# Kernel tuning notes

Measured on AMD Instinct MI355X. Metric: run time of the kernel, lower is better.

The kernel has to match this reference:

```python
import jax, jax.numpy as jnp
import numpy as np

QMIN, QMAX = 0.0, 255.0  # uint8 activation quantization range


def _qlinear(x, w_q, b, s_in, zp_in, s_w):
    """zentorch_qlinear: quantize fp32 x to uint8, int8 weight, dequant output.

    x:   [M, K] fp32
    w_q: [N, K] int8 values (stored int32), symmetric (weight zp = 0)
    b:   [N] fp32
    s_in, zp_in: scalars (activation scale / zero point)
    s_w: [N] per-output-channel weight scales
    """
    zp = zp_in.astype(jnp.float32)
    q = jnp.clip(jnp.round(x / s_in) + zp, QMIN, QMAX)      # fake-quant uint8
    x_dq = (q - zp) * s_in                                   # dequantized activation
    w_dq = w_q.astype(jnp.float32) * s_w[:, None]            # [N, K] dequant weight
    return x_dq @ w_dq.T + b                                 # [M, N] fp32


def setup_inputs() -> dict:
    key = jax.random.key(0)
    k1, k2, k3, k4 = jax.random.split(key, 4)
    M, K, N = 8192, 4096, 4096
    inp = {
        "input": jax.random.normal(k1, (M, K), dtype=jnp.float32),
        "weights": jax.random.randint(k2, (N, K), -128, 128, dtype=jnp.int32),
        "biases": jax.random.normal(k3, (N,), dtype=jnp.float32) * 0.1,
        "input_scales": jnp.array([0.05], dtype=jnp.float32),
        "input_zero_points": jnp.array([128], dtype=jnp.int32),
        "weight_scales": jax.random.uniform(k4, (N,), dtype=jnp.float32, minval=0.001, maxval=0.01),
        "weight_zero_points": jnp.zeros((N,), dtype=jnp.int32),
        "output_dtype": 0,  # 0 -> float32
    }
    return inp


def reference(input, weights, biases, input_scales, input_zero_points,
              weight_scales, weight_zero_points, output_dtype):
    s_in = input_scales[0]
    zp_in = input_zero_points[0]
    x = _qlinear(input, weights, biases, s_in, zp_in, weight_scales)
    x = _qlinear(x, weights, biases, s_in, zp_in, weight_scales)
    x = _qlinear(x, weights, biases, s_in, zp_in, weight_scales)
    return x
```

## Files before the change

### kernel.cpp

```cpp
#include <hip/hip_runtime.h>
#include <stdint.h>

#define M_DIM 8192
#define K_DIM 4096
#define N_DIM 4096
#define KTILES (K_DIM / 64)

typedef __attribute__((ext_vector_type(4))) int i32x4;

__global__ void pack_w_kernel(const int* __restrict__ w, char* __restrict__ wp,
                              int* __restrict__ corr, const int* __restrict__ zpp) {
  __shared__ int red[256];
  const int n = blockIdx.x;
  const int t = threadIdx.x;
  const int4* row = (const int4*)(w + (size_t)n * K_DIM);
  int s = 0;
  int words[4];
#pragma unroll
  for (int u = 0; u < 4; ++u) {
    int4 v = row[t * 4 + u];
    s += v.x + v.y + v.z + v.w;
    words[u] = (v.x & 255) | ((v.y & 255) << 8) | ((v.z & 255) << 16) | (v.w << 24);
  }
  ((int4*)(wp + (size_t)n * K_DIM))[t] = make_int4(words[0], words[1], words[2], words[3]);
  red[t] = s;
  __syncthreads();
  for (int off = 128; off > 0; off >>= 1) {
    if (t < off) red[t] += red[t + off];
    __syncthreads();
  }
  if (t == 0) corr[n] = (128 - zpp[0]) * red[0];
}

__global__ void quant_in_kernel(const float* __restrict__ x, char* __restrict__ q,
                                const float* __restrict__ sp, const int* __restrict__ zpp) {
  const int i = blockIdx.x * blockDim.x + threadIdx.x;
  const float s = sp[0];
  const float zp = (float)zpp[0];
  float4 v = ((const float4*)x)[i];
  float t0 = fminf(fmaxf(rintf(v.x / s) + zp, 0.f), 255.f);
  float t1 = fminf(fmaxf(rintf(v.y / s) + zp, 0.f), 255.f);
  float t2 = fminf(fmaxf(rintf(v.z / s) + zp, 0.f), 255.f);
  float t3 = fminf(fmaxf(rintf(v.w / s) + zp, 0.f), 255.f);
  int b0 = (int)t0 - 128, b1 = (int)t1 - 128, b2 = (int)t2 - 128, b3 = (int)t3 - 128;
  ((int*)q)[i] = (b0 & 255) | ((b1 & 255) << 8) | ((b2 & 255) << 16) | (b3 << 24);
}

#define STAGE16(SRC, DST)                                                     \
  __builtin_amdgcn_global_load_lds(                                           \
      (const __attribute__((address_space(1))) void*)(SRC),                   \
      (__attribute__((address_space(3))) void*)(DST), 16, 0, 0)

#define RD(p) (*(const i32x4*)(p))

#define TILE4(SLOT, KS)                                                       \
  {                                                                           \
    const char* cA_ = &lds[SLOT][0][0];                                       \
    const char* cB_ = &lds[SLOT][1][0];                                       \
    char* nA_ = &lds[((SLOT) + 3) & 3][0][0];                                 \
    char* nB_ = &lds[((SLOT) + 3) & 3][1][0];                                 \
    i32x4 a_[4], b_[4];                                                       \
    _Pragma("unroll") for (int i_ = 0; i_ < 4; ++i_)                          \
        a_[i_] = RD(cA_ + aoff[i_]);                                          \
    _Pragma("unroll") for (int j_ = 0; j_ < 4; ++j_)                          \
        b_[j_] = RD(cB_ + boff[j_]);                                          \
    STAGE16(asrc0 + (size_t)(KS), nA_ + o0_);                                 \
    STAGE16(bsrc0 + (size_t)(KS), nB_ + o0_);                                 \
    __builtin_amdgcn_s_setprio(1);                                            \
    _Pragma("unroll") for (int i_ = 0; i_ < 4; ++i_)                          \
        _Pragma("unroll") for (int j_ = 0; j_ < 4; ++j_)                      \
            acc[i_][j_] = __builtin_amdgcn_mfma_i32_16x16x64_i8(              \
                a_[i_], b_[j_], acc[i_][j_], 0, 0, 0);                        \
    __builtin_amdgcn_s_setprio(0);                                            \
    asm volatile("s_waitcnt vmcnt(2)" ::: "memory");                          \
    __builtin_amdgcn_s_barrier();                                             \
  }

template <int WRITE_Q>
__global__ __launch_bounds__(1024, 4) void gemm_kernel(
    const char* __restrict__ qa, const char* __restrict__ wb,
    const int* __restrict__ corr, const float* __restrict__ swp,
    const float* __restrict__ bias, const float* __restrict__ sp,
    const int* __restrict__ zpp, char* __restrict__ outq, float* __restrict__ outf) {
  __shared__ __align__(16) char lds[4][2][16384];
  const int tid = threadIdx.x;
  const int lane = tid & 63;
  const int w = tid >> 6;
  const int wr = w >> 2;
  const int wc = w & 3;
  const int bid = blockIdx.x;
  const int bm = bid & 31;
  const int bn = bid >> 5;
  const char* abase = qa + (size_t)bm * 256 * K_DIM;
  const char* bbase = wb + (size_t)bn * 256 * K_DIM;

  const int o0_ = tid * 16;
  const int r0_ = tid >> 2;
  const int sl_ = tid & 3;
  const int g0_ = sl_ ^ ((r0_ >> 1) & 3);
  const char* asrc0 = abase + (size_t)r0_ * K_DIM + g0_ * 16;
  const int p0_ = (r0_ & ~63) + 4 * (r0_ & 15) + ((r0_ >> 4) & 3);
  const char* bsrc0 = bbase + (size_t)p0_ * K_DIM + g0_ * 16;

  const int rr = lane & 15;
  const int g = lane >> 4;
  int aoff[4], boff[4];
#pragma unroll
  for (int i = 0; i < 4; ++i) {
    const int rowA = wr * 64 + i * 16 + rr;
    aoff[i] = (rowA << 6) + ((g ^ ((rowA >> 1) & 3)) << 4);
    const int rowB = wc * 64 + i * 16 + rr;
    boff[i] = (rowB << 6) + ((g ^ ((rowB >> 1) & 3)) << 4);
  }

  i32x4 acc[4][4] = {};

  STAGE16(asrc0, &lds[0][0][o0_]);       STAGE16(bsrc0, &lds[0][1][o0_]);
  STAGE16(asrc0 + 64, &lds[1][0][o0_]);  STAGE16(bsrc0 + 64, &lds[1][1][o0_]);
  STAGE16(asrc0 + 128, &lds[2][0][o0_]); STAGE16(bsrc0 + 128, &lds[2][1][o0_]);
  asm volatile("s_waitcnt vmcnt(2)" ::: "memory");
  __builtin_amdgcn_s_barrier();

#define KCL(x) ((size_t)((x) < KTILES ? (x) : KTILES - 1) * 64)
  for (int tb = 0; tb < KTILES / 4; ++tb) {
    const int t0 = tb * 4;
    TILE4(0, KCL(t0 + 3))
    TILE4(1, KCL(t0 + 4))
    TILE4(2, KCL(t0 + 5))
    TILE4(3, KCL(t0 + 6))
  }
#undef KCL
  asm volatile("s_waitcnt vmcnt(0)" ::: "memory");

  const float s = sp[0];
  const float zpf = (float)zpp[0];
  const int m0 = bm * 256 + wr * 64 + (lane >> 4) * 4;
  const int nb4 = bn * 256 + wc * 64 + ((lane & 15) << 2);
  const int4 cr4 = *(const int4*)(corr + nb4);
  const float4 sw4 = *(const float4*)(swp + nb4);
  const float4 bb4 = *(const float4*)(bias + nb4);
  const float fs0 = s * sw4.x, fs1 = s * sw4.y, fs2 = s * sw4.z, fs3 = s * sw4.w;
#pragma unroll
  for (int i = 0; i < 4; ++i) {
#pragma unroll
    for (int q = 0; q < 4; ++q) {
      const int m = m0 + i * 16 + q;
      const float v0 = fs0 * (float)(acc[i][0][q] + cr4.x) + bb4.x;
      const float v1 = fs1 * (float)(acc[i][1][q] + cr4.y) + bb4.y;
      const float v2 = fs2 * (float)(acc[i][2][q] + cr4.z) + bb4.z;
      const float v3 = fs3 * (float)(acc[i][3][q] + cr4.w) + bb4.w;
      if (WRITE_Q) {
        const int b0i = (int)fminf(fmaxf(rintf(v0 / s) + zpf, 0.f), 255.f) - 128;
        const int b1i = (int)fminf(fmaxf(rintf(v1 / s) + zpf, 0.f), 255.f) - 128;
        const int b2i = (int)fminf(fmaxf(rintf(v2 / s) + zpf, 0.f), 255.f) - 128;
        const int b3i = (int)fminf(fmaxf(rintf(v3 / s) + zpf, 0.f), 255.f) - 128;
        const uint32_t pk = (uint32_t)(b0i & 255) | ((uint32_t)(b1i & 255) << 8) |
                            ((uint32_t)(b2i & 255) << 16) | ((uint32_t)b3i << 24);
        *(uint32_t*)(outq + (size_t)m * N_DIM + nb4) = pk;
      } else {
        float4 o4;
        o4.x = v0; o4.y = v1; o4.z = v2; o4.w = v3;
        *(float4*)(outf + (size_t)m * N_DIM + nb4) = o4;
      }
    }
  }
}

extern "C" void kernel_launch(void* const* d_in, const int* in_sizes, int n_in,
                              void* d_out, int out_size, void* d_ws, size_t ws_size,
                              hipStream_t stream) {
  const float* x = (const float*)d_in[0];
  const int* wq = (const int*)d_in[1];
  const float* bias = (const float*)d_in[2];
  const float* s_in = (const float*)d_in[3];
  const int* zp_in = (const int*)d_in[4];
  const float* s_w = (const float*)d_in[5];
  float* out = (float*)d_out;

  const size_t WP_BYTES = (size_t)N_DIM * K_DIM;
  const size_t Q_BYTES = (size_t)M_DIM * K_DIM;
  char* ws = (char*)d_ws;
  char* wp = ws;
  char* q1 = ws + WP_BYTES;
  char* q2 = q1 + Q_BYTES;
  int* corr = (int*)(q2 + Q_BYTES);
  const size_t NEEDED = WP_BYTES + 2 * Q_BYTES + (size_t)N_DIM * sizeof(int);
  if (ws_size < NEEDED) return;

  pack_w_kernel<<<N_DIM, 256, 0, stream>>>(wq, wp, corr, zp_in);
  quant_in_kernel<<<(M_DIM * K_DIM / 4) / 256, 256, 0, stream>>>(x, q1, s_in, zp_in);

  dim3 grid((M_DIM / 256) * (N_DIM / 256));
  dim3 blk(1024);
  gemm_kernel<1><<<grid, blk, 0, stream>>>(q1, wp, corr, s_w, bias, s_in, zp_in, q2, nullptr);
  gemm_kernel<1><<<grid, blk, 0, stream>>>(q2, wp, corr, s_w, bias, s_in, zp_in, q1, nullptr);
  gemm_kernel<0><<<grid, blk, 0, stream>>>(q1, wp, corr, s_w, bias, s_in, zp_in, nullptr, out);
}
```

Measured before the change: 438.0 us.

## Shrink GEMM tile to 256x128 with 512 threads and 3-stage LDS ring

Measured after the change: 489.4 us. +11.8%, slower.

```diff
diff --git a/kernel.cpp b/kernel.cpp
--- a/kernel.cpp
+++ b/kernel.cpp
@@ -53,54 +53,57 @@
 
 #define RD(p) (*(const i32x4*)(p))
 
-#define TILE4(SLOT, KS)                                                       \
+#define TILE3(SLOT, KS)                                                       \
   {                                                                           \
-    const char* cA_ = &lds[SLOT][0][0];                                       \
-    const char* cB_ = &lds[SLOT][1][0];                                       \
-    char* nA_ = &lds[((SLOT) + 3) & 3][0][0];                                 \
-    char* nB_ = &lds[((SLOT) + 3) & 3][1][0];                                 \
+    const char* c_ = lds + (SLOT) * 24576;                                    \
+    char* nx_ = lds + (((SLOT) + 2) % 3) * 24576;                             \
     i32x4 a_[4], b_[4];                                                       \
     _Pragma("unroll") for (int i_ = 0; i_ < 4; ++i_)                          \
-        a_[i_] = RD(cA_ + aoff[i_]);                                          \
+        a_[i_] = RD(c_ + aoff[i_]);                                           \
     _Pragma("unroll") for (int j_ = 0; j_ < 4; ++j_)                          \
-        b_[j_] = RD(cB_ + boff[j_]);                                          \
-    STAGE16(asrc0 + (size_t)(KS), nA_ + o0_);                                 \
-    STAGE16(bsrc0 + (size_t)(KS), nB_ + o0_);                                 \
+        b_[j_] = RD(c_ + boff[j_]);                                           \
+    STAGE16(asr0 + (size_t)(KS), nx_ + oa0);                                  \
+    STAGE16(asr1 + (size_t)(KS), nx_ + oa1);                                  \
+    STAGE16(bsr0 + (size_t)(KS), nx_ + ob0);                                  \
     __builtin_amdgcn_s_setprio(1);                                            \
     _Pragma("unroll") for (int i_ = 0; i_ < 4; ++i_)                          \
         _Pragma("unroll") for (int j_ = 0; j_ < 4; ++j_)                      \
             acc[i_][j_] = __builtin_amdgcn_mfma_i32_16x16x64_i8(              \
                 a_[i_], b_[j_], acc[i_][j_], 0, 0, 0);                        \
     __builtin_amdgcn_s_setprio(0);                                            \
-    asm volatile("s_waitcnt vmcnt(2)" ::: "memory");                          \
+    asm volatile("s_waitcnt vmcnt(3)" ::: "memory");                          \
     __builtin_amdgcn_s_barrier();                                             \
   }
 
 template <int WRITE_Q>
-__global__ __launch_bounds__(1024, 4) void gemm_kernel(
+__global__ __launch_bounds__(512, 4) void gemm_kernel(
     const char* __restrict__ qa, const char* __restrict__ wb,
     const int* __restrict__ corr, const float* __restrict__ swp,
     const float* __restrict__ bias, const float* __restrict__ sp,
     const int* __restrict__ zpp, char* __restrict__ outq, float* __restrict__ outf) {
-  __shared__ __align__(16) char lds[4][2][16384];
+  __shared__ __align__(16) char lds[3 * 24576];
   const int tid = threadIdx.x;
   const int lane = tid & 63;
   const int w = tid >> 6;
-  const int wr = w >> 2;
-  const int wc = w & 3;
+  const int wr = w >> 1;
+  const int wc = w & 1;
   const int bid = blockIdx.x;
   const int bm = bid & 31;
   const int bn = bid >> 5;
   const char* abase = qa + (size_t)bm * 256 * K_DIM;
-  const char* bbase = wb + (size_t)bn * 256 * K_DIM;
-
-  const int o0_ = tid * 16;
-  const int r0_ = tid >> 2;
+  const char* bbase = wb + (size_t)bn * 128 * K_DIM;
+
+  const int oa0 = tid * 16;
+  const int oa1 = 8192 + tid * 16;
+  const int ob0 = 16384 + tid * 16;
   const int sl_ = tid & 3;
-  const int g0_ = sl_ ^ ((r0_ >> 1) & 3);
-  const char* asrc0 = abase + (size_t)r0_ * K_DIM + g0_ * 16;
-  const int p0_ = (r0_ & ~63) + 4 * (r0_ & 15) + ((r0_ >> 4) & 3);
-  const char* bsrc0 = bbase + (size_t)p0_ * K_DIM + g0_ * 16;
+  const int ra0 = (tid * 16) >> 6;
+  const int ra1 = (8192 + tid * 16) >> 6;
+  const int rb0 = (tid * 16) >> 6;
+  const char* asr0 = abase + (size_t)ra0 * K_DIM + (sl_ ^ ((ra0 >> 1) & 3)) * 16;
+  const char* asr1 = abase + (size_t)ra1 * K_DIM + (sl_ ^ ((ra1 >> 1) & 3)) * 16;
+  const int pb0 = (rb0 & ~63) + 4 * (rb0 & 15) + ((rb0 >> 4) & 3);
+  const char* bsr0 = bbase + (size_t)pb0 * K_DIM + (sl_ ^ ((rb0 >> 1) & 3)) * 16;
 
   const int rr = lane & 15;
   const int g = lane >> 4;
@@ -110,32 +113,33 @@
     const int rowA = wr * 64 + i * 16 + rr;
     aoff[i] = (rowA << 6) + ((g ^ ((rowA >> 1) & 3)) << 4);
     const int rowB = wc * 64 + i * 16 + rr;
-    boff[i] = (rowB << 6) + ((g ^ ((rowB >> 1) & 3)) << 4);
+    boff[i] = 16384 + (rowB << 6) + ((g ^ ((rowB >> 1) & 3)) << 4);
   }
 
   i32x4 acc[4][4] = {};
 
-  STAGE16(asrc0, &lds[0][0][o0_]);       STAGE16(bsrc0, &lds[0][1][o0_]);
-  STAGE16(asrc0 + 64, &lds[1][0][o0_]);  STAGE16(bsrc0 + 64, &lds[1][1][o0_]);
-  STAGE16(asrc0 + 128, &lds[2][0][o0_]); STAGE16(bsrc0 + 128, &lds[2][1][o0_]);
-  asm volatile("s_waitcnt vmcnt(2)" ::: "memory");
+  STAGE16(asr0, lds + oa0); STAGE16(asr1, lds + oa1); STAGE16(bsr0, lds + ob0);
+  STAGE16(asr0 + 64, lds + 24576 + oa0);
+  STAGE16(asr1 + 64, lds + 24576 + oa1);
+  STAGE16(bsr0 + 64, lds + 24576 + ob0);
+  asm volatile("s_waitcnt vmcnt(3)" ::: "memory");
   __builtin_amdgcn_s_barrier();
 
 #define KCL(x) ((size_t)((x) < KTILES ? (x) : KTILES - 1) * 64)
-  for (int tb = 0; tb < KTILES / 4; ++tb) {
-    const int t0 = tb * 4;
-    TILE4(0, KCL(t0 + 3))
-    TILE4(1, KCL(t0 + 4))
-    TILE4(2, KCL(t0 + 5))
-    TILE4(3, KCL(t0 + 6))
-  }
+  for (int t3 = 0; t3 < 21; ++t3) {
+    const int t0 = t3 * 3;
+    TILE3(0, KCL(t0 + 2))
+    TILE3(1, KCL(t0 + 3))
+    TILE3(2, KCL(t0 + 4))
+  }
+  TILE3(0, KCL(KTILES - 1))
 #undef KCL
   asm volatile("s_waitcnt vmcnt(0)" ::: "memory");
 
   const float s = sp[0];
   const float zpf = (float)zpp[0];
   const int m0 = bm * 256 + wr * 64 + (lane >> 4) * 4;
-  const int nb4 = bn * 256 + wc * 64 + ((lane & 15) << 2);
+  const int nb4 = bn * 128 + wc * 64 + ((lane & 15) << 2);
   const int4 cr4 = *(const int4*)(corr + nb4);
   const float4 sw4 = *(const float4*)(swp + nb4);
   const float4 bb4 = *(const float4*)(bias + nb4);
@@ -190,8 +194,8 @@
   pack_w_kernel<<<N_DIM, 256, 0, stream>>>(wq, wp, corr, zp_in);
   quant_in_kernel<<<(M_DIM * K_DIM / 4) / 256, 256, 0, stream>>>(x, q1, s_in, zp_in);
 
-  dim3 grid((M_DIM / 256) * (N_DIM / 256));
-  dim3 blk(1024);
+  dim3 grid((M_DIM / 256) * (N_DIM / 128));
+  dim3 blk(512);
   gemm_kernel<1><<<grid, blk, 0, stream>>>(q1, wp, corr, s_w, bias, s_in, zp_in, q2, nullptr);
   gemm_kernel<1><<<grid, blk, 0, stream>>>(q2, wp, corr, s_w, bias, s_in, zp_in, q1, nullptr);
   gemm_kernel<0><<<grid, blk, 0, stream>>>(q1, wp, corr, s_w, bias, s_in, zp_in, nullptr, out);
```

## Load B operand directly into registers from MFMA-prepacked weight layout

Applied to the files above, without the earlier changes.

New measurement: 449.3 us. 1.03x slower.

```diff
diff --git a/kernel.cpp b/kernel.cpp
--- a/kernel.cpp
+++ b/kernel.cpp
@@ -13,16 +13,21 @@
   __shared__ int red[256];
   const int n = blockIdx.x;
   const int t = threadIdx.x;
-  const int4* row = (const int4*)(w + (size_t)n * K_DIM);
+  const int kt = t >> 2;
+  const int g = t & 3;
+  const int* row = w + (size_t)n * K_DIM + kt * 64 + g * 16;
   int s = 0;
   int words[4];
 #pragma unroll
   for (int u = 0; u < 4; ++u) {
-    int4 v = row[t * 4 + u];
+    int4 v = *(const int4*)(row + u * 4);
     s += v.x + v.y + v.z + v.w;
     words[u] = (v.x & 255) | ((v.y & 255) << 8) | ((v.z & 255) << 16) | (v.w << 24);
   }
-  ((int4*)(wp + (size_t)n * K_DIM))[t] = make_int4(words[0], words[1], words[2], words[3]);
+  const int j = n & 3;
+  const int r = (n & 63) >> 2;
+  char* dst = wp + ((size_t)(n >> 6) * 64 + kt) * 4096 + j * 1024 + (g * 16 + r) * 16;
+  *(int4*)dst = make_int4(words[0], words[1], words[2], words[3]);
   red[t] = s;
   __syncthreads();
   for (int off = 128; off > 0; off >>= 1) {
@@ -53,36 +58,37 @@
 
 #define RD(p) (*(const i32x4*)(p))
 
-#define TILE4(SLOT, KS)                                                       \
+#define TILEB(SLOT, KSTG, TBN, BC, BN_, DO_NEXT)                              \
   {                                                                           \
-    const char* cA_ = &lds[SLOT][0][0];                                       \
-    const char* cB_ = &lds[SLOT][1][0];                                       \
-    char* nA_ = &lds[((SLOT) + 3) & 3][0][0];                                 \
-    char* nB_ = &lds[((SLOT) + 3) & 3][1][0];                                 \
-    i32x4 a_[4], b_[4];                                                       \
+    const char* cA_ = &lds[SLOT][0];                                          \
+    char* nA_ = &lds[((SLOT) + 3) & 3][0];                                    \
+    i32x4 a_[4];                                                              \
     _Pragma("unroll") for (int i_ = 0; i_ < 4; ++i_)                          \
         a_[i_] = RD(cA_ + aoff[i_]);                                          \
-    _Pragma("unroll") for (int j_ = 0; j_ < 4; ++j_)                          \
-        b_[j_] = RD(cB_ + boff[j_]);                                          \
-    STAGE16(asrc0 + (size_t)(KS), nA_ + o0_);                                 \
-    STAGE16(bsrc0 + (size_t)(KS), nB_ + o0_);                                 \
+    if (DO_NEXT) {                                                            \
+      _Pragma("unroll") for (int j_ = 0; j_ < 4; ++j_)                        \
+          BN_[j_] = RD(bbase + (size_t)(TBN) * 4096 + j_ * 1024);             \
+      STAGE16(asrc0 + (size_t)(KSTG) * 64, nA_ + o0_);                        \
+      asm volatile("s_waitcnt vmcnt(5)" ::: "memory");                        \
+    } else {                                                                  \
+      asm volatile("s_waitcnt vmcnt(0)" ::: "memory");                        \
+    }                                                                         \
+    __builtin_amdgcn_s_barrier();                                             \
     __builtin_amdgcn_s_setprio(1);                                            \
     _Pragma("unroll") for (int i_ = 0; i_ < 4; ++i_)                          \
         _Pragma("unroll") for (int j_ = 0; j_ < 4; ++j_)                      \
             acc[i_][j_] = __builtin_amdgcn_mfma_i32_16x16x64_i8(              \
-                a_[i_], b_[j_], acc[i_][j_], 0, 0, 0);                        \
+                a_[i_], BC[j_], acc[i_][j_], 0, 0, 0);                        \
     __builtin_amdgcn_s_setprio(0);                                            \
-    asm volatile("s_waitcnt vmcnt(2)" ::: "memory");                          \
-    __builtin_amdgcn_s_barrier();                                             \
   }
 
 template <int WRITE_Q>
 __global__ __launch_bounds__(1024, 4) void gemm_kernel(
-    const char* __restrict__ qa, const char* __restrict__ wb,
+    const char* __restrict__ qa, const char* __restrict__ wbp,
     const int* __restrict__ corr, const float* __restrict__ swp,
     const float* __restrict__ bias, const float* __restrict__ sp,
     const int* __restrict__ zpp, char* __restrict__ outq, float* __restrict__ outf) {
-  __shared__ __align__(16) char lds[4][2][16384];
+  __shared__ __align__(16) char lds[4][16384];
   const int tid = threadIdx.x;
   const int lane = tid & 63;
   const int w = tid >> 6;
@@ -92,45 +98,46 @@
   const int bm = bid & 31;
   const int bn = bid >> 5;
   const char* abase = qa + (size_t)bm * 256 * K_DIM;
-  const char* bbase = wb + (size_t)bn * 256 * K_DIM;
 
   const int o0_ = tid * 16;
   const int r0_ = tid >> 2;
   const int sl_ = tid & 3;
   const int g0_ = sl_ ^ ((r0_ >> 1) & 3);
   const char* asrc0 = abase + (size_t)r0_ * K_DIM + g0_ * 16;
-  const int p0_ = (r0_ & ~63) + 4 * (r0_ & 15) + ((r0_ >> 4) & 3);
-  const char* bsrc0 = bbase + (size_t)p0_ * K_DIM + g0_ * 16;
+
+  const char* bbase = wbp + (size_t)(bn * 4 + wc) * 262144 + lane * 16;
 
   const int rr = lane & 15;
   const int g = lane >> 4;
-  int aoff[4], boff[4];
+  int aoff[4];
 #pragma unroll
   for (int i = 0; i < 4; ++i) {
     const int rowA = wr * 64 + i * 16 + rr;
     aoff[i] = (rowA << 6) + ((g ^ ((rowA >> 1) & 3)) << 4);
-    const int rowB = wc * 64 + i * 16 + rr;
-    boff[i] = (rowB << 6) + ((g ^ ((rowB >> 1) & 3)) << 4);
   }
 
   i32x4 acc[4][4] = {};
-
-  STAGE16(asrc0, &lds[0][0][o0_]);       STAGE16(bsrc0, &lds[0][1][o0_]);
-  STAGE16(asrc0 + 64, &lds[1][0][o0_]);  STAGE16(bsrc0 + 64, &lds[1][1][o0_]);
-  STAGE16(asrc0 + 128, &lds[2][0][o0_]); STAGE16(bsrc0 + 128, &lds[2][1][o0_]);
+  i32x4 bA[4], bB[4];
+
+  STAGE16(asrc0, &lds[0][o0_]);
+#pragma unroll
+  for (int j = 0; j < 4; ++j) bA[j] = RD(bbase + j * 1024);
+  STAGE16(asrc0 + 64, &lds[1][o0_]);
+  STAGE16(asrc0 + 128, &lds[2][o0_]);
   asm volatile("s_waitcnt vmcnt(2)" ::: "memory");
   __builtin_amdgcn_s_barrier();
 
-#define KCL(x) ((size_t)((x) < KTILES ? (x) : KTILES - 1) * 64)
-  for (int tb = 0; tb < KTILES / 4; ++tb) {
+  for (int tb = 0; tb < 15; ++tb) {
     const int t0 = tb * 4;
-    TILE4(0, KCL(t0 + 3))
-    TILE4(1, KCL(t0 + 4))
-    TILE4(2, KCL(t0 + 5))
-    TILE4(3, KCL(t0 + 6))
-  }
-#undef KCL
-  asm volatile("s_waitcnt vmcnt(0)" ::: "memory");
+    TILEB(0, t0 + 3, t0 + 1, bA, bB, 1)
+    TILEB(1, t0 + 4, t0 + 2, bB, bA, 1)
+    TILEB(2, t0 + 5, t0 + 3, bA, bB, 1)
+    TILEB(3, t0 + 6, t0 + 4, bB, bA, 1)
+  }
+  TILEB(0, KTILES - 1, 61, bA, bB, 1)
+  TILEB(1, KTILES - 1, 62, bB, bA, 1)
+  TILEB(2, KTILES - 1, 63, bA, bB, 1)
+  TILEB(3, 0, 0, bB, bA, 0)
 
   const float s = sp[0];
   const float zpf = (float)zpp[0];
```
